# Kernel optimization log

Measured on AMD Instinct MI355X. Metric: run time of the kernel, lower is better.

Reference implementation:

```python
import jax, jax.numpy as jnp
import numpy as np

VOCAB, EMBED, CONV_C, HID, LABELS = 50257, 512, 512, 1024, 128
B, S = 32, 1024

def setup_inputs() -> dict:
    key = jax.random.key(0)
    ks = jax.random.split(key, 8)
    sc = lambda d: 1.0 / np.sqrt(d)
    return {
        "token_ids": jax.random.randint(ks[0], (B, S), 0, VOCAB),
        "emb_table": jax.random.normal(ks[1], (VOCAB, EMBED), jnp.float32) * 0.02,
        "conv_w": jax.random.normal(ks[2], (CONV_C, EMBED), jnp.float32) * sc(EMBED),
        "conv_b": jnp.zeros((CONV_C,), jnp.float32),
        "dec_w1": jax.random.normal(ks[3], (CONV_C, HID), jnp.float32) * sc(CONV_C),
        "dec_b1": jnp.zeros((HID,), jnp.float32),
        "dec_w2": jax.random.normal(ks[4], (HID, LABELS), jnp.float32) * sc(HID),
        "dec_b2": jnp.zeros((LABELS,), jnp.float32),
    }

def reference(token_ids, emb_table, conv_w, conv_b, dec_w1, dec_b1, dec_w2, dec_b2):
    # Embedding lookup: [B, S, E]
    x = emb_table[token_ids]
    # DocNN encoder on a length-1 sequence = kernel-1 conv + relu (+ trivial max-over-time)
    h = jax.nn.relu(jnp.einsum('bse,ce->bsc', x, conv_w) + conv_b)  # [B,S,C]
    # MLP decoder per word
    z = jax.nn.relu(jnp.einsum('bsc,ch->bsh', h, dec_w1) + dec_b1)  # [B,S,H]
    logits = jnp.einsum('bsh,hl->bsl', z, dec_w2) + dec_b2          # [B,S,L]
    # torch.cat over dim 0 of per-word outputs -> flat [B*S, L]
    return logits.reshape(-1, logits.shape[-1])
```

## Files before the change

kernel.cpp:

```cpp
#include <hip/hip_runtime.h>

typedef __bf16 bf16;
typedef __bf16 bf16x4 __attribute__((ext_vector_type(4)));
typedef __bf16 bf16x8 __attribute__((ext_vector_type(8)));
typedef float f32x4 __attribute__((ext_vector_type(4)));

#define NROWS 32768
#define EMBED 512
#define CONV_C 512
#define HID 1024
#define LABELS 128

__device__ inline void async16(const void* g, void* l) {
  __builtin_amdgcn_global_load_lds(
      (const __attribute__((address_space(1))) void*)g,
      (__attribute__((address_space(3))) void*)l, 16, 0, 0);
}

__device__ inline int swap4(int x) { return ((x >> 2) | ((x & 3) << 2)) & 15; }
__device__ inline int bitswap02(int g) {
  return ((g & 1) << 2) | (g & 0xA) | ((g >> 2) & 1);
}

__device__ inline bf16x8 cvt8_sw(const float* row, int o0, int o1) {
  f32x4 lo = *(const f32x4*)(row + o0);
  f32x4 hi = *(const f32x4*)(row + o1);
  bf16x8 r;
  r[0] = (bf16)lo[0]; r[1] = (bf16)lo[1]; r[2] = (bf16)lo[2]; r[3] = (bf16)lo[3];
  r[4] = (bf16)hi[0]; r[5] = (bf16)hi[1]; r[6] = (bf16)hi[2]; r[7] = (bf16)hi[3];
  return r;
}


__global__ void cvt_bf16(const float* __restrict__ in, bf16* __restrict__ out, int n) {
  int i = (blockIdx.x * blockDim.x + threadIdx.x) * 4;
  if (i >= n) return;
  float4 v = *(const float4*)(in + i);
  bf16x4 o;
  o.x = (bf16)v.x; o.y = (bf16)v.y; o.z = (bf16)v.z; o.w = (bf16)v.w;
  *(bf16x4*)(out + i) = o;
}

__global__ void transpose_cvt(const float* __restrict__ in, bf16* __restrict__ out,
                              int K, int N) {
  __shared__ float t[64][65];
  int kb = blockIdx.x * 64, nb = blockIdx.y * 64;
  for (int i = threadIdx.x; i < 4096; i += 256) {
    int r = i >> 6, c = i & 63;
    t[r][c] = in[(size_t)(kb + r) * N + nb + c];
  }
  __syncthreads();
  for (int i = threadIdx.x; i < 4096; i += 256) {
    int r = i >> 6, c = i & 63;
    out[(size_t)(nb + r) * K + kb + c] = (bf16)t[c][r];
  }
}

__global__ __launch_bounds__(256) void gemm1_gather(
    const int* __restrict__ tok, const float* __restrict__ emb,
    const bf16* __restrict__ convw, const float* __restrict__ bias,
    bf16* __restrict__ out, int M, int N, int K) {
  __shared__ __attribute__((aligned(16))) char smem[49152];
  const int tid = threadIdx.x;
  const int wave = tid >> 6, lane = tid & 63;
  const int m0 = blockIdx.x * 128, n0 = blockIdx.y * 128;
  const int wm = (wave & 1) * 64, wn = (wave >> 1) * 64;
  const int lrow = lane & 15, quad = lane >> 4;
  const int slot0 = wave * 64 + lane;

  int arow[4], acol[4];
#pragma unroll
  for (int c = 0; c < 4; ++c) {
    int s = slot0 + c * 256;
    int r = s >> 3, p = s & 7;
    arow[c] = r;
    acol[c] = (p ^ (r & 7)) * 4;
  }
  int trow[4];
#pragma unroll
  for (int c = 0; c < 4; ++c) trow[c] = tok[m0 + arow[c]];

  const f32x4 zero4 = {0.f, 0.f, 0.f, 0.f};
  f32x4 acc[4][4];
#pragma unroll
  for (int i = 0; i < 4; ++i)
#pragma unroll
    for (int j = 0; j < 4; ++j) acc[i][j] = zero4;

  auto stage = [&](int p, int k0) {
    float* lAf = (float*)(smem + p * 24576);
    bf16* lB = (bf16*)(smem + p * 24576 + 16384);
#pragma unroll
    for (int c = 0; c < 4; ++c)
      async16(emb + (size_t)trow[c] * EMBED + k0 + acol[c],
              lAf + (size_t)(wave * 64 + c * 256) * 4);
#pragma unroll
    for (int c = 0; c < 2; ++c) {
      int s = slot0 + c * 256;
      int r = s >> 2, cs = s & 3;
      async16(convw + (size_t)(n0 + r) * K + k0 + cs * 8,
              lB + (size_t)(wave * 64 + c * 256) * 8);
    }
  };

  stage(0, 0);
  int cur = 0;
  for (int it = 0; it < 16; ++it) {
    __syncthreads();
    if (it < 15) stage(cur ^ 1, (it + 1) * 32);
    const float* lAf = (const float*)(smem + cur * 24576);
    const bf16* lB = (const bf16*)(smem + cur * 24576 + 16384);

    bf16x8 a[4], b[4];
#pragma unroll
    for (int t = 0; t < 4; ++t) {
      int r = wm + t * 16 + lrow, sw = r & 7;
      a[t] = cvt8_sw(lAf + r * 32, ((2 * quad) ^ sw) * 4, ((2 * quad + 1) ^ sw) * 4);
      b[t] = *(const bf16x8*)(lB + (wn + t * 16 + lrow) * 32 + quad * 8);
    }
#pragma unroll
    for (int mi = 0; mi < 4; ++mi)
#pragma unroll
      for (int ni = 0; ni < 4; ++ni)
        acc[mi][ni] =
            __builtin_amdgcn_mfma_f32_16x16x32_bf16(a[mi], b[ni], acc[mi][ni], 0, 0, 0);
    cur ^= 1;
  }

#pragma unroll
  for (int mi = 0; mi < 4; ++mi) {
#pragma unroll
    for (int ni = 0; ni < 4; ++ni) {
      int col = n0 + wn + ni * 16 + lrow;
      float bv = bias[col];
#pragma unroll
      for (int r = 0; r < 4; ++r) {
        int row = m0 + wm + mi * 16 + quad * 4 + r;
        float v = acc[mi][ni][r] + bv;
        v = v > 0.f ? v : 0.f;
        out[(size_t)row * N + col] = (bf16)v;
      }
    }
  }
}

__global__ __launch_bounds__(256) void gemm23_fused(
    const bf16* __restrict__ h,
    const bf16* __restrict__ w1t,
    const bf16* __restrict__ w2t,
    const float* __restrict__ b1, const float* __restrict__ b2,
    float* __restrict__ out) {
  __shared__ __attribute__((aligned(16))) char smem[81920];
  bf16* zbuf = (bf16*)smem;
  bf16* lB3 = (bf16*)(smem + 49152);
  const int tid = threadIdx.x, wave = tid >> 6, lane = tid & 63;
  const int m0 = blockIdx.x * 64;
  const int wm = (wave & 1) * 32, wn = (wave >> 1) * 64;
  const int lrow = lane & 15, quad = lane >> 4;
  const int slot0 = wave * 64 + lane;
  const int sw_lrow = swap4(lrow);

  int a_r[2], a_c[2];
#pragma unroll
  for (int c = 0; c < 2; ++c) {
    int s = slot0 + c * 256;
    a_r[c] = s >> 3;
    a_c[c] = ((s & 7) ^ (a_r[c] & 7)) * 8;
  }
  int b_r[4], b_c[4];
#pragma unroll
  for (int c = 0; c < 4; ++c) {
    int s = slot0 + c * 256;
    b_r[c] = s >> 3;
    b_c[c] = ((s & 7) ^ (b_r[c] & 7)) * 8;
  }
  int w2_r[8], w2_c[8];
#pragma unroll
  for (int c = 0; c < 8; ++c) {
    int s = slot0 + c * 256;
    w2_r[c] = s >> 4;
    w2_c[c] = bitswap02((s & 15) ^ swap4(w2_r[c] & 15)) * 8;
  }

  auto stage = [&](int p, const bf16* wB, int k0) {
    bf16* lA = (bf16*)(smem + p * 24576);
    bf16* lB = (bf16*)(smem + p * 24576 + 8192);
#pragma unroll
    for (int c = 0; c < 2; ++c)
      async16(h + (size_t)(m0 + a_r[c]) * 512 + k0 + a_c[c],
              lA + (size_t)(wave * 64 + c * 256) * 8);
#pragma unroll
    for (int c = 0; c < 4; ++c)
      async16(wB + (size_t)b_r[c] * 512 + k0 + b_c[c],
              lB + (size_t)(wave * 64 + c * 256) * 8);
  };

  const f32x4 zero4 = {0.f, 0.f, 0.f, 0.f};
  f32x4 out_acc[2][4];
#pragma unroll
  for (int i = 0; i < 2; ++i)
#pragma unroll
    for (int j = 0; j < 4; ++j) out_acc[i][j] = zero4;

  for (int chunk = 0; chunk < 8; ++chunk) {
    f32x4 z_acc[2][4];
#pragma unroll
    for (int i = 0; i < 2; ++i)
#pragma unroll
      for (int j = 0; j < 4; ++j) z_acc[i][j] = zero4;

    const bf16* wB = w1t + (size_t)(chunk * 128) * 512;

#pragma unroll
    for (int c = 0; c < 8; ++c)
      async16(w2t + (size_t)w2_r[c] * HID + chunk * 128 + w2_c[c],
              lB3 + (size_t)(wave * 64 + c * 256) * 8);
    stage(0, wB, 0);

    int cur = 0;
    for (int it = 0; it < 8; ++it) {
      __syncthreads();
      if (it < 7) stage(cur ^ 1, wB, (it + 1) * 64);
      const bf16* lA = (const bf16*)(smem + cur * 24576);
      const bf16* lB = (const bf16*)(smem + cur * 24576 + 8192);

#pragma unroll
      for (int ks = 0; ks < 2; ++ks) {
        bf16x8 a[2], b[4];
#pragma unroll
        for (int t = 0; t < 2; ++t) {
          int row = wm + t * 16 + lrow;
          int pos = (ks * 4 + quad) ^ (row & 7);
          a[t] = *(const bf16x8*)(lA + row * 64 + pos * 8);
        }
#pragma unroll
        for (int t = 0; t < 4; ++t) {
          int row = wn + t * 16 + lrow;
          int pos = (ks * 4 + quad) ^ (row & 7);
          b[t] = *(const bf16x8*)(lB + row * 64 + pos * 8);
        }
#pragma unroll
        for (int mi = 0; mi < 2; ++mi)
#pragma unroll
          for (int ni = 0; ni < 4; ++ni)
            z_acc[mi][ni] =
                __builtin_amdgcn_mfma_f32_16x16x32_bf16(a[mi], b[ni], z_acc[mi][ni], 0, 0, 0);
      }
      cur ^= 1;
    }
#pragma unroll
    for (int mi = 0; mi < 2; ++mi) {
#pragma unroll
      for (int ni = 0; ni < 4; ++ni) {
        int col = wn + ni * 16 + lrow;
        float bv = b1[chunk * 128 + col];
        int gsw = bitswap02(col >> 3);
#pragma unroll
        for (int r = 0; r < 4; ++r) {
          int row = wm + mi * 16 + quad * 4 + r;
          float v = z_acc[mi][ni][r] + bv;
          v = v > 0.f ? v : 0.f;
          int pos = gsw ^ (quad | (r << 2));
          zbuf[row * 128 + pos * 8 + (col & 7)] = (bf16)v;
        }
      }
    }
    __syncthreads();

#pragma unroll
    for (int ks = 0; ks < 4; ++ks) {
      int possw = bitswap02(ks * 4 + quad) ^ sw_lrow;
      bf16x8 a3[2], b3[4];
#pragma unroll
      for (int mi = 0; mi < 2; ++mi) {
        int row = wm + mi * 16 + lrow;
        a3[mi] = *(const bf16x8*)(zbuf + row * 128 + possw * 8);
      }
#pragma unroll
      for (int ni = 0; ni < 4; ++ni) {
        int row = wn + ni * 16 + lrow;
        b3[ni] = *(const bf16x8*)(lB3 + row * 128 + possw * 8);
      }
#pragma unroll
      for (int mi = 0; mi < 2; ++mi)
#pragma unroll
        for (int ni = 0; ni < 4; ++ni)
          out_acc[mi][ni] =
              __builtin_amdgcn_mfma_f32_16x16x32_bf16(a3[mi], b3[ni], out_acc[mi][ni], 0, 0, 0);
    }
    __syncthreads();
  }

#pragma unroll
  for (int mi = 0; mi < 2; ++mi) {
#pragma unroll
    for (int ni = 0; ni < 4; ++ni) {
      int col = wn + ni * 16 + lrow;
      float bv = b2[col];
#pragma unroll
      for (int r = 0; r < 4; ++r) {
        int row = m0 + wm + mi * 16 + quad * 4 + r;
        out[(size_t)row * LABELS + col] = out_acc[mi][ni][r] + bv;
      }
    }
  }
}


extern "C" void kernel_launch(void* const* d_in, const int* in_sizes, int n_in,
                              void* d_out, int out_size, void* d_ws, size_t ws_size,
                              hipStream_t stream) {
  const int* tok = (const int*)d_in[0];
  const float* emb = (const float*)d_in[1];
  const float* conv_w = (const float*)d_in[2];
  const float* conv_b = (const float*)d_in[3];
  const float* w1 = (const float*)d_in[4];
  const float* b1 = (const float*)d_in[5];
  const float* w2 = (const float*)d_in[6];
  const float* b2 = (const float*)d_in[7];
  float* out = (float*)d_out;

  char* ws = (char*)d_ws;
  bf16* wtc = (bf16*)(ws);
  bf16* wt1 = (bf16*)(ws + (1u << 19));
  bf16* wt2 = (bf16*)(ws + 3 * (1u << 19));
  bf16* h = (bf16*)(ws + (2u << 20));

  hipLaunchKernelGGL(cvt_bf16, dim3(256), dim3(256), 0, stream,
                     conv_w, wtc, CONV_C * EMBED);
  hipLaunchKernelGGL(transpose_cvt, dim3(8, 16), dim3(256), 0, stream,
                     w1, wt1, CONV_C, HID);
  hipLaunchKernelGGL(transpose_cvt, dim3(16, 2), dim3(256), 0, stream,
                     w2, wt2, HID, LABELS);

  hipLaunchKernelGGL(gemm1_gather, dim3(NROWS / 128, CONV_C / 128), dim3(256),
                     0, stream, tok, emb, wtc, conv_b, h, NROWS, CONV_C, EMBED);
  hipLaunchKernelGGL(gemm23_fused, dim3(NROWS / 64), dim3(256),
                     0, stream, h, wt1, wt2, b1, b2, out);
}
```

Before: 253.5 us.

## Enlarge fused decoder tile to 128 rows and pipeline layer-3 weight staging

Reworks the fused second and third GEMM kernel to use 512-thread blocks covering 128 rows. The hidden dimension is now processed in 256-wide chunks instead of 128, so each staged tile feeds more MFMAs and the activations and W1 are re-read fewer times. The W2 slices are double-buffered in 64-wide pieces and interleaved with the layer-3 MFMAs, and the next chunk's activation tile is prefetched during layer 3. The z buffer reuses the W1 staging region. The cost is 128KB of LDS per block, which allows at most one block per CU, and higher register pressure from the larger accumulator arrays.

```diff
diff --git a/kernel.cpp b/kernel.cpp
--- a/kernel.cpp
+++ b/kernel.cpp
@@ -17,7 +17,6 @@
       (__attribute__((address_space(3))) void*)l, 16, 0, 0);
 }
 
-__device__ inline int swap4(int x) { return ((x >> 2) | ((x & 3) << 2)) & 15; }
 __device__ inline int bitswap02(int g) {
   return ((g & 1) << 2) | (g & 0xA) | ((g >> 2) & 1);
 }
@@ -144,103 +143,133 @@
   }
 }
 
-__global__ __launch_bounds__(256) void gemm23_fused(
+__global__ __launch_bounds__(512, 2) void gemm23_fused(
     const bf16* __restrict__ h,
     const bf16* __restrict__ w1t,
     const bf16* __restrict__ w2t,
     const float* __restrict__ b1, const float* __restrict__ b2,
     float* __restrict__ out) {
-  __shared__ __attribute__((aligned(16))) char smem[81920];
-  bf16* zbuf = (bf16*)smem;
-  bf16* lB3 = (bf16*)(smem + 49152);
+  __shared__ __attribute__((aligned(16))) char smem[131072];
+  bf16* zbuf = (bf16*)(smem + 32768);
   const int tid = threadIdx.x, wave = tid >> 6, lane = tid & 63;
-  const int m0 = blockIdx.x * 64;
-  const int wm = (wave & 1) * 32, wn = (wave >> 1) * 64;
+  const int m0 = blockIdx.x * 128;
+  const int am0 = (wave >> 2) * 64;
+  const int bn0 = (wave & 3) * 64;
+  const int lb0 = (wave & 3) * 32;
   const int lrow = lane & 15, quad = lane >> 4;
-  const int slot0 = wave * 64 + lane;
-  const int sw_lrow = swap4(lrow);
+  const int lsw = lrow & 7;
+  const int bsw = bitswap02(lsw);
 
   int a_r[2], a_c[2];
 #pragma unroll
   for (int c = 0; c < 2; ++c) {
-    int s = slot0 + c * 256;
+    int s = tid + c * 512;
     a_r[c] = s >> 3;
     a_c[c] = ((s & 7) ^ (a_r[c] & 7)) * 8;
   }
   int b_r[4], b_c[4];
 #pragma unroll
   for (int c = 0; c < 4; ++c) {
-    int s = slot0 + c * 256;
+    int s = tid + c * 512;
     b_r[c] = s >> 3;
     b_c[c] = ((s & 7) ^ (b_r[c] & 7)) * 8;
   }
-  int w2_r[8], w2_c[8];
-#pragma unroll
-  for (int c = 0; c < 8; ++c) {
-    int s = slot0 + c * 256;
-    w2_r[c] = s >> 4;
-    w2_c[c] = bitswap02((s & 15) ^ swap4(w2_r[c] & 15)) * 8;
-  }
-
-  auto stage = [&](int p, const bf16* wB, int k0) {
-    bf16* lA = (bf16*)(smem + p * 24576);
-    bf16* lB = (bf16*)(smem + p * 24576 + 8192);
+  int q_r[2], q_c[2];
+#pragma unroll
+  for (int c = 0; c < 2; ++c) {
+    int s = tid + c * 512;
+    q_r[c] = s >> 3;
+    q_c[c] = ((s & 7) ^ (q_r[c] & 7)) * 8;
+  }
+
+  auto stageA = [&](int p, int k0) {
+    bf16* lA = (bf16*)(smem + p * 16384);
 #pragma unroll
     for (int c = 0; c < 2; ++c)
       async16(h + (size_t)(m0 + a_r[c]) * 512 + k0 + a_c[c],
-              lA + (size_t)(wave * 64 + c * 256) * 8);
+              lA + (size_t)(tid + c * 512) * 8);
+  };
+  auto stageB = [&](int p, int cn0, int k0) {
+    bf16* lB = (bf16*)(smem + 32768 + p * 32768);
 #pragma unroll
     for (int c = 0; c < 4; ++c)
-      async16(wB + (size_t)b_r[c] * 512 + k0 + b_c[c],
-              lB + (size_t)(wave * 64 + c * 256) * 8);
+      async16(w1t + (size_t)(cn0 + b_r[c]) * 512 + k0 + b_c[c],
+              lB + (size_t)(tid + c * 512) * 8);
+  };
+  auto stageQ = [&](int cn0, int qq, int pq) {
+    bf16* lQ = (bf16*)(smem + 98304 + pq * 16384);
+#pragma unroll
+    for (int c = 0; c < 2; ++c)
+      async16(w2t + (size_t)q_r[c] * HID + cn0 + qq * 64 + q_c[c],
+              lQ + (size_t)(tid + c * 512) * 8);
   };
 
   const f32x4 zero4 = {0.f, 0.f, 0.f, 0.f};
-  f32x4 out_acc[2][4];
-#pragma unroll
-  for (int i = 0; i < 2; ++i)
-#pragma unroll
-    for (int j = 0; j < 4; ++j) out_acc[i][j] = zero4;
-
-  for (int chunk = 0; chunk < 8; ++chunk) {
-    f32x4 z_acc[2][4];
-#pragma unroll
-    for (int i = 0; i < 2; ++i)
+  f32x4 out_acc[4][2];
+#pragma unroll
+  for (int i = 0; i < 4; ++i)
+#pragma unroll
+    for (int j = 0; j < 2; ++j) out_acc[i][j] = zero4;
+
+  auto layer3 = [&](int qq, int pq) {
+    const bf16* lQ = (const bf16*)(smem + 98304 + pq * 16384);
+#pragma unroll
+    for (int ks = 0; ks < 2; ++ks) {
+      bf16x8 a3[4], b3[2];
+#pragma unroll
+      for (int t = 0; t < 4; ++t) {
+        int m = am0 + t * 16 + lrow;
+        int kq = qq * 8 + ks * 4 + quad;
+        a3[t] = *(const bf16x8*)(zbuf + m * 256 + ((kq ^ bsw) << 3));
+      }
+#pragma unroll
+      for (int t = 0; t < 2; ++t) {
+        int lab = lb0 + t * 16 + lrow;
+        b3[t] = *(const bf16x8*)(lQ + lab * 64 + (((ks * 4 + quad) ^ lsw) * 8));
+      }
+#pragma unroll
+      for (int mi = 0; mi < 4; ++mi)
+#pragma unroll
+        for (int ni = 0; ni < 2; ++ni)
+          out_acc[mi][ni] =
+              __builtin_amdgcn_mfma_f32_16x16x32_bf16(a3[mi], b3[ni], out_acc[mi][ni], 0, 0, 0);
+    }
+  };
+
+  for (int chunk = 0; chunk < 4; ++chunk) {
+    const int cn0 = chunk * 256;
+    if (chunk == 0) stageA(0, 0);
+    stageB(0, cn0, 0);
+    stageQ(cn0, 0, 0);
+
+    f32x4 z_acc[4][4];
+#pragma unroll
+    for (int i = 0; i < 4; ++i)
 #pragma unroll
       for (int j = 0; j < 4; ++j) z_acc[i][j] = zero4;
-
-    const bf16* wB = w1t + (size_t)(chunk * 128) * 512;
-
-#pragma unroll
-    for (int c = 0; c < 8; ++c)
-      async16(w2t + (size_t)w2_r[c] * HID + chunk * 128 + w2_c[c],
-              lB3 + (size_t)(wave * 64 + c * 256) * 8);
-    stage(0, wB, 0);
 
     int cur = 0;
     for (int it = 0; it < 8; ++it) {
       __syncthreads();
-      if (it < 7) stage(cur ^ 1, wB, (it + 1) * 64);
-      const bf16* lA = (const bf16*)(smem + cur * 24576);
-      const bf16* lB = (const bf16*)(smem + cur * 24576 + 8192);
-
+      if (it < 7) {
+        stageB(cur ^ 1, cn0, (it + 1) * 64);
+        stageA(cur ^ 1, (it + 1) * 64);
+      }
+      const bf16* lA = (const bf16*)(smem + cur * 16384);
+      const bf16* lB = (const bf16*)(smem + 32768 + cur * 32768);
 #pragma unroll
       for (int ks = 0; ks < 2; ++ks) {
-        bf16x8 a[2], b[4];
-#pragma unroll
-        for (int t = 0; t < 2; ++t) {
-          int row = wm + t * 16 + lrow;
-          int pos = (ks * 4 + quad) ^ (row & 7);
-          a[t] = *(const bf16x8*)(lA + row * 64 + pos * 8);
-        }
-#pragma unroll
-        for (int t = 0; t < 4; ++t) {
-          int row = wn + t * 16 + lrow;
-          int pos = (ks * 4 + quad) ^ (row & 7);
-          b[t] = *(const bf16x8*)(lB + row * 64 + pos * 8);
-        }
-#pragma unroll
-        for (int mi = 0; mi < 2; ++mi)
+        bf16x8 a[4], b[4];
+#pragma unroll
+        for (int t = 0; t < 4; ++t)
+          a[t] = *(const bf16x8*)(lA + (am0 + t * 16 + lrow) * 64 +
+                                  (((ks * 4 + quad) ^ lsw) * 8));
+#pragma unroll
+        for (int t = 0; t < 4; ++t)
+          b[t] = *(const bf16x8*)(lB + (bn0 + t * 16 + lrow) * 64 +
+                                  (((ks * 4 + quad) ^ lsw) * 8));
+#pragma unroll
+        for (int mi = 0; mi < 4; ++mi)
 #pragma unroll
           for (int ni = 0; ni < 4; ++ni)
             z_acc[mi][ni] =
@@ -248,58 +277,48 @@
       }
       cur ^= 1;
     }
-#pragma unroll
-    for (int mi = 0; mi < 2; ++mi) {
+
+    __syncthreads();
+    stageQ(cn0, 1, 1);
+#pragma unroll
+    for (int mi = 0; mi < 4; ++mi) {
 #pragma unroll
       for (int ni = 0; ni < 4; ++ni) {
-        int col = wn + ni * 16 + lrow;
-        float bv = b1[chunk * 128 + col];
-        int gsw = bitswap02(col >> 3);
+        int zcol = bn0 + ni * 16 + lrow;
+        float bv = b1[cn0 + zcol];
+        int q5 = zcol >> 3;
 #pragma unroll
         for (int r = 0; r < 4; ++r) {
-          int row = wm + mi * 16 + quad * 4 + r;
+          int zrow = am0 + mi * 16 + quad * 4 + r;
           float v = z_acc[mi][ni][r] + bv;
           v = v > 0.f ? v : 0.f;
-          int pos = gsw ^ (quad | (r << 2));
-          zbuf[row * 128 + pos * 8 + (col & 7)] = (bf16)v;
+          zbuf[zrow * 256 + ((q5 ^ bitswap02(zrow & 7)) << 3) + (zcol & 7)] = (bf16)v;
         }
       }
     }
     __syncthreads();
-
-#pragma unroll
-    for (int ks = 0; ks < 4; ++ks) {
-      int possw = bitswap02(ks * 4 + quad) ^ sw_lrow;
-      bf16x8 a3[2], b3[4];
-#pragma unroll
-      for (int mi = 0; mi < 2; ++mi) {
-        int row = wm + mi * 16 + lrow;
-        a3[mi] = *(const bf16x8*)(zbuf + row * 128 + possw * 8);
-      }
-#pragma unroll
-      for (int ni = 0; ni < 4; ++ni) {
-        int row = wn + ni * 16 + lrow;
-        b3[ni] = *(const bf16x8*)(lB3 + row * 128 + possw * 8);
-      }
-#pragma unroll
-      for (int mi = 0; mi < 2; ++mi)
-#pragma unroll
-        for (int ni = 0; ni < 4; ++ni)
-          out_acc[mi][ni] =
-              __builtin_amdgcn_mfma_f32_16x16x32_bf16(a3[mi], b3[ni], out_acc[mi][ni], 0, 0, 0);
-    }
-    __syncthreads();
-  }
-
-#pragma unroll
-  for (int mi = 0; mi < 2; ++mi) {
-#pragma unroll
-    for (int ni = 0; ni < 4; ++ni) {
-      int col = wn + ni * 16 + lrow;
+    layer3(0, 0);
+    __syncthreads();
+    stageQ(cn0, 2, 0);
+    layer3(1, 1);
+    __syncthreads();
+    stageQ(cn0, 3, 1);
+    if (chunk < 3) stageA(0, 0);
+    layer3(2, 0);
+    __syncthreads();
+    layer3(3, 1);
+    __syncthreads();
+  }
+
+#pragma unroll
+  for (int mi = 0; mi < 4; ++mi) {
+#pragma unroll
+    for (int ni = 0; ni < 2; ++ni) {
+      int col = lb0 + ni * 16 + lrow;
       float bv = b2[col];
 #pragma unroll
       for (int r = 0; r < 4; ++r) {
-        int row = m0 + wm + mi * 16 + quad * 4 + r;
+        int row = m0 + am0 + mi * 16 + quad * 4 + r;
         out[(size_t)row * LABELS + col] = out_acc[mi][ni][r] + bv;
       }
     }
@@ -335,6 +354,6 @@
 
   hipLaunchKernelGGL(gemm1_gather, dim3(NROWS / 128, CONV_C / 128), dim3(256),
                      0, stream, tok, emb, wtc, conv_b, h, NROWS, CONV_C, EMBED);
-  hipLaunchKernelGGL(gemm23_fused, dim3(NROWS / 64), dim3(256),
+  hipLaunchKernelGGL(gemm23_fused, dim3(NROWS / 128), dim3(512),
                      0, stream, h, wt1, wt2, b1, b2, out);
 }
```

New measurement: 242.7 us. -4.2%, faster.
